# Performance work log

Hardware: AMD Instinct MI355X
Metric: run time of the kernel (lower is better)

The kernel has to match this reference:

```python
import math
import jax, jax.numpy as jnp
import numpy as np

E = 1024
H = 16
D = E // H  # head_dim = 64
B, T = 4, 2048


def setup_inputs() -> dict:
    key = jax.random.key(0)
    ks = jax.random.split(key, 9)
    s = 1.0 / math.sqrt(E)
    inp = {
        "x": jax.random.normal(ks[0], (B, T, E), dtype=jnp.float32),
        "Wq": jax.random.uniform(ks[1], (E, E), jnp.float32, -s, s),
        "bq": jax.random.uniform(ks[2], (E,), jnp.float32, -s, s),
        "Wk": jax.random.uniform(ks[3], (E, E), jnp.float32, -s, s),
        "bk": jax.random.uniform(ks[4], (E,), jnp.float32, -s, s),
        "Wv": jax.random.uniform(ks[5], (E, E), jnp.float32, -s, s),
        "bv": jax.random.uniform(ks[6], (E,), jnp.float32, -s, s),
        "Wo": jax.random.uniform(ks[7], (E, E), jnp.float32, -s, s),
        "bo": jax.random.uniform(ks[8], (E,), jnp.float32, -s, s),
    }
    return inp


def reference(x, Wq, bq, Wk, bk, Wv, bv, Wo, bo):
    # Linear projections (torch Linear: y = x @ W.T + b)
    q = x @ Wq.T + bq
    k = x @ Wk.T + bk
    v = x @ Wv.T + bv
    # [B, T, E] -> [B, H, T, D]
    def split_heads(t):
        return t.reshape(B, T, H, D).transpose(0, 2, 1, 3)
    q, k, v = split_heads(q), split_heads(k), split_heads(v)
    # scaled dot-product attention; note scale uses head_dim (attention(self.head_dim))
    scores = jnp.einsum("bhqd,bhkd->bhqk", q, k) / math.sqrt(D)
    attn = jax.nn.softmax(scores, axis=-1)
    out = jnp.einsum("bhqk,bhkd->bhqd", attn, v)
    out = out.transpose(0, 2, 1, 3).reshape(B, T, E)
    return out @ Wo.T + bo
```

## Files before the change

kernel.cpp:

```cpp
#include <hip/hip_runtime.h>

typedef short bh8 __attribute__((ext_vector_type(8)));
typedef short bh4 __attribute__((ext_vector_type(4)));
typedef float f4 __attribute__((ext_vector_type(4)));
typedef unsigned int u32;
typedef u32 u32x2 __attribute__((ext_vector_type(2)));

#if __has_builtin(__builtin_amdgcn_exp2f)
#define EXP2(x) __builtin_amdgcn_exp2f(x)
#else
#define EXP2(x) exp2f(x)
#endif

__device__ __forceinline__ short f2bf(float f) {
  unsigned u = __float_as_uint(f);
  u += 0x7FFFu + ((u >> 16) & 1u);
  return (short)(u >> 16);
}

__device__ __forceinline__ void async16(const void* g, void* l) {
  __builtin_amdgcn_global_load_lds((const __attribute__((address_space(1))) void*)g,
                                   (__attribute__((address_space(3))) void*)l, 16, 0, 0);
}

__global__ void cvt_kernel(const float* __restrict__ in, short* __restrict__ out, int n4) {
  int i = blockIdx.x * blockDim.x + threadIdx.x;
  if (i < n4) {
    f4 v = *(const f4*)(in + (size_t)i * 4);
    bh4 o;
    o[0] = f2bf(v[0]); o[1] = f2bf(v[1]); o[2] = f2bf(v[2]); o[3] = f2bf(v[3]);
    *(bh4*)(out + (size_t)i * 4) = o;
  }
}

__global__ void cvt_w4(const float* __restrict__ w0, const float* __restrict__ w1,
                       const float* __restrict__ w2, const float* __restrict__ w3,
                       short* __restrict__ out, int n4_per) {
  const float* in = blockIdx.y == 0 ? w0 : blockIdx.y == 1 ? w1 : blockIdx.y == 2 ? w2 : w3;
  short* o = out + (size_t)blockIdx.y * (size_t)n4_per * 4;
  int i = blockIdx.x * blockDim.x + threadIdx.x;
  if (i < n4_per) {
    f4 v = *(const f4*)(in + (size_t)i * 4);
    bh4 q;
    q[0] = f2bf(v[0]); q[1] = f2bf(v[1]); q[2] = f2bf(v[2]); q[3] = f2bf(v[3]);
    *(bh4*)(o + (size_t)i * 4) = q;
  }
}

template <typename OutT, bool BROW>
__device__ __forceinline__ void gemm_body(const short* __restrict__ A, const short* __restrict__ Bw,
                                          const float* __restrict__ bias, OutT* __restrict__ C,
                                          int m0, int n0, int N, int K, float scale,
                                          short* a_lds, short* b_lds) {
  const int t = threadIdx.x;
  const int lane = t & 63, wave = t >> 6, quad = lane >> 4, l15 = lane & 15;
  const int mw = (wave >> 1) * 64, nw = (wave & 1) * 64;

  f4 acc[4][4];
#pragma unroll
  for (int i = 0; i < 4; ++i)
#pragma unroll
    for (int j = 0; j < 4; ++j) acc[i][j] = (f4){0.f, 0.f, 0.f, 0.f};

  for (int k0 = 0; k0 < K; k0 += 32) {
#pragma unroll
    for (int i = 0; i < 2; ++i) {
      int c = i * 256 + t;
      int m = c >> 2;
      int kq = (c & 3) ^ ((m >> 1) & 3);
      const short* ga = A + (size_t)(m0 + m) * K + k0 + kq * 8;
      const short* gb = Bw + (size_t)(n0 + m) * K + k0 + kq * 8;
      async16(ga, (char*)a_lds + (i * 256 + wave * 64) * 16);
      async16(gb, (char*)b_lds + (i * 256 + wave * 64) * 16);
    }
    __syncthreads();
    bh8 af[4], bfr[4];
#pragma unroll
    for (int ms = 0; ms < 4; ++ms) {
      int m = mw + ms * 16 + l15;
      int pos = m * 4 + (quad ^ ((m >> 1) & 3));
      af[ms] = *(const bh8*)(a_lds + pos * 8);
    }
#pragma unroll
    for (int ns = 0; ns < 4; ++ns) {
      int n = nw + ns * 16 + l15;
      int pos = n * 4 + (quad ^ ((n >> 1) & 3));
      bfr[ns] = *(const bh8*)(b_lds + pos * 8);
    }
#pragma unroll
    for (int ms = 0; ms < 4; ++ms)
#pragma unroll
      for (int ns = 0; ns < 4; ++ns)
        acc[ms][ns] = __builtin_amdgcn_mfma_f32_16x16x32_bf16(af[ms], bfr[ns], acc[ms][ns], 0, 0, 0);
    __syncthreads();
  }
#pragma unroll
  for (int ns = 0; ns < 4; ++ns) {
    int col = n0 + nw + ns * 16 + l15;
    float bcol = BROW ? 0.f : bias[col & 1023];
#pragma unroll
    for (int ms = 0; ms < 4; ++ms) {
      int row = m0 + mw + ms * 16 + quad * 4;
      float brow = BROW ? bias[row & 1023] : 0.f;
#pragma unroll
      for (int r = 0; r < 4; ++r) {
        float bv = BROW ? bias[(row + r) & 1023] : bcol;
        float v = (acc[ms][ns][r] + bv) * scale;
        if (sizeof(OutT) == 2)
          ((short*)C)[(size_t)(row + r) * N + col] = f2bf(v);
        else
          ((float*)C)[(size_t)(row + r) * N + col] = v;
      }
      (void)brow;
    }
  }
}

__global__ void gemm_qkv(const short* __restrict__ xb, const short* __restrict__ W3,
                         const float* __restrict__ bq, const float* __restrict__ bk,
                         const float* __restrict__ bv,
                         short* __restrict__ Qo, short* __restrict__ Ko, short* __restrict__ VTo,
                         float qscale) {
  __shared__ __align__(16) short a_lds[128 * 32];
  __shared__ __align__(16) short b_lds[128 * 32];
  const int which = blockIdx.x >> 3;
  if (which == 2) {
    const short* Wv = W3 + (size_t)2 * 1024 * 1024;
    gemm_body<short, true>(Wv, xb, bv, VTo, (blockIdx.x & 7) * 128, blockIdx.y * 128,
                           8192, 1024, 1.0f, a_lds, b_lds);
  } else {
    const short* Bw = W3 + (size_t)which * 1024 * 1024;
    const float* bias = which == 0 ? bq : bk;
    short* C = which == 0 ? Qo : Ko;
    float scale = which == 0 ? qscale : 1.0f;
    gemm_body<short, false>(xb, Bw, bias, C, blockIdx.y * 128, (blockIdx.x & 7) * 128,
                            1024, 1024, scale, a_lds, b_lds);
  }
}

__global__ void gemm_bt_f32(const short* __restrict__ A, const short* __restrict__ Bw,
                            const float* __restrict__ bias, float* __restrict__ C) {
  __shared__ __align__(16) short a_lds[128 * 32];
  __shared__ __align__(16) short b_lds[128 * 32];
  gemm_body<float, false>(A, Bw, bias, C, blockIdx.y * 128, blockIdx.x * 128, 1024, 1024, 1.0f,
                          a_lds, b_lds);
}

__global__ void attn_kernel(const short* __restrict__ Qb, const short* __restrict__ Kb,
                            const short* __restrict__ VTb, short* __restrict__ AO) {
  __shared__ __align__(16) short k_lds[64 * 64];
  __shared__ __align__(16) short vt_lds[64 * 64];
  __shared__ __align__(16) short p_lds[4][32 * 72];
  const int t = threadIdx.x, lane = t & 63, wave = t >> 6, quad = lane >> 4, l15 = lane & 15;
  const int bh = blockIdx.y, b = bh >> 4, h = bh & 15;
  const int q0 = blockIdx.x * 128;
  const size_t baseq = ((size_t)b * 2048) * 1024 + (size_t)h * 64;
  const size_t basev = ((size_t)h * 64) * 8192 + (size_t)b * 2048;

  bh8 qf[2][2];
#pragma unroll
  for (int mi = 0; mi < 2; ++mi)
#pragma unroll
    for (int ks = 0; ks < 2; ++ks)
      qf[mi][ks] = *(const bh8*)(Qb + baseq + (size_t)(q0 + wave * 32 + mi * 16 + l15) * 1024 + ks * 32 + quad * 8);

  f4 O[2][4];
  float l_part[2] = {0.f, 0.f};
#pragma unroll
  for (int mi = 0; mi < 2; ++mi)
#pragma unroll
    for (int di = 0; di < 4; ++di) O[mi][di] = (f4){0.f, 0.f, 0.f, 0.f};

  for (int kt = 0; kt < 2048; kt += 64) {
    __syncthreads();
#pragma unroll
    for (int i = 0; i < 2; ++i) {
      int c = i * 256 + t;
      int kk = c >> 3;
      int dq = (c & 7) ^ (kk & 7);
      async16(Kb + baseq + (size_t)(kt + kk) * 1024 + dq * 8,
              (char*)k_lds + (i * 256 + wave * 64) * 16);
    }
#pragma unroll
    for (int i = 0; i < 2; ++i) {
      int c = i * 256 + t;
      int d = c >> 3;
      int kc = (c & 7) ^ (d & 7);
      async16(VTb + basev + (size_t)d * 8192 + kt + kc * 8,
              (char*)vt_lds + (i * 256 + wave * 64) * 16);
    }
    __syncthreads();

    f4 ST[4][2];
#pragma unroll
    for (int mK = 0; mK < 4; ++mK) {
      int key = mK * 16 + l15;
      bh8 ka0 = *(const bh8*)(k_lds + (key * 8 + (quad ^ (key & 7))) * 8);
      bh8 ka1 = *(const bh8*)(k_lds + (key * 8 + ((quad + 4) ^ (key & 7))) * 8);
#pragma unroll
      for (int mi = 0; mi < 2; ++mi) {
        f4 s = (f4){-16.f, -16.f, -16.f, -16.f};
        s = __builtin_amdgcn_mfma_f32_16x16x32_bf16(ka0, qf[mi][0], s, 0, 0, 0);
        s = __builtin_amdgcn_mfma_f32_16x16x32_bf16(ka1, qf[mi][1], s, 0, 0, 0);
        ST[mK][mi] = s;
      }
    }

#pragma unroll
    for (int mi = 0; mi < 2; ++mi) {
      float lp = 0.f;
#pragma unroll
      for (int mK = 0; mK < 4; ++mK) {
        float p0 = EXP2(ST[mK][mi][0]);
        float p1 = EXP2(ST[mK][mi][1]);
        float p2 = EXP2(ST[mK][mi][2]);
        float p3 = EXP2(ST[mK][mi][3]);
        lp += (p0 + p1) + (p2 + p3);
        u32 d0 = __builtin_amdgcn_perm(__float_as_uint(p1), __float_as_uint(p0), 0x07060302u);
        u32 d1 = __builtin_amdgcn_perm(__float_as_uint(p3), __float_as_uint(p2), 0x07060302u);
        u32x2 dd = {d0, d1};
        *(u32x2*)(&p_lds[wave][(mi * 16 + l15) * 72 + mK * 16 + quad * 4]) = dd;
      }
      l_part[mi] += lp;
    }

    bh8 pa[2][2];
#pragma unroll
    for (int mi = 0; mi < 2; ++mi)
#pragma unroll
      for (int ks = 0; ks < 2; ++ks)
        pa[mi][ks] = *(const bh8*)(&p_lds[wave][(mi * 16 + l15) * 72 + ks * 32 + quad * 8]);
#pragma unroll
    for (int di = 0; di < 4; ++di) {
      int d = di * 16 + l15;
      bh8 vb0 = *(const bh8*)(vt_lds + (d * 8 + (quad ^ (d & 7))) * 8);
      bh8 vb1 = *(const bh8*)(vt_lds + (d * 8 + ((quad + 4) ^ (d & 7))) * 8);
#pragma unroll
      for (int mi = 0; mi < 2; ++mi) {
        f4 o = O[mi][di];
        o = __builtin_amdgcn_mfma_f32_16x16x32_bf16(pa[mi][0], vb0, o, 0, 0, 0);
        o = __builtin_amdgcn_mfma_f32_16x16x32_bf16(pa[mi][1], vb1, o, 0, 0, 0);
        O[mi][di] = o;
      }
    }
  }

#pragma unroll
  for (int mi = 0; mi < 2; ++mi) {
    float l0 = l_part[mi];
    l0 += __shfl_xor(l0, 16);
    l0 += __shfl_xor(l0, 32);
    float rl[4];
#pragma unroll
    for (int r = 0; r < 4; ++r) {
      float lb = __shfl(l0, quad * 4 + r);
      rl[r] = __builtin_amdgcn_rcpf(lb);
    }
#pragma unroll
    for (int di = 0; di < 4; ++di)
#pragma unroll
      for (int r = 0; r < 4; ++r) {
        int row = q0 + wave * 32 + mi * 16 + quad * 4 + r;
        AO[baseq + (size_t)row * 1024 + di * 16 + l15] = f2bf(O[mi][di][r] * rl[r]);
      }
  }
}

extern "C" void kernel_launch(void* const* d_in, const int* in_sizes, int n_in,
                              void* d_out, int out_size, void* d_ws, size_t ws_size,
                              hipStream_t stream) {
  const float* x  = (const float*)d_in[0];
  const float* Wq = (const float*)d_in[1];
  const float* bq = (const float*)d_in[2];
  const float* Wk = (const float*)d_in[3];
  const float* bk = (const float*)d_in[4];
  const float* Wv = (const float*)d_in[5];
  const float* bv = (const float*)d_in[6];
  const float* Wo = (const float*)d_in[7];
  const float* bo = (const float*)d_in[8];
  float* out = (float*)d_out;

  const int M = 8192, E = 1024;
  const size_t NX = (size_t)M * E;
  const size_t NW = (size_t)E * E;

  short* ws  = (short*)d_ws;
  short* xb  = ws;
  short* wqb = xb + NX;
  short* wob = wqb + 3 * NW;
  short* qb  = wob + NW;
  short* kb  = qb + NX;
  short* vt  = kb + NX;
  short* aob = xb;

  cvt_kernel<<<dim3((unsigned)(NX / 1024)), 256, 0, stream>>>(x, xb, (int)(NX / 4));
  cvt_w4<<<dim3((unsigned)(NW / 1024), 4), 256, 0, stream>>>(Wq, Wk, Wv, Wo, wqb, (int)(NW / 4));

  const float qscale = 0.18033688011112042f;
  gemm_qkv<<<dim3(24, 64), 256, 0, stream>>>(xb, wqb, bq, bk, bv, qb, kb, vt, qscale);

  attn_kernel<<<dim3(16, 64), 256, 0, stream>>>(qb, kb, vt, aob);

  gemm_bt_f32<<<dim3(8, 64), 256, 0, stream>>>(aob, wob, bo, out);
}
```

Before: 281.6 us.

## Keep softmax probabilities in registers via f16 MFMA and double GEMM K-tile

The attention kernel now converts exp2 probabilities to packed fp16 in registers and feeds them straight into 16x16x16 f16 MFMAs, so the per-wave LDS round trip for P is gone. To match that, V is stored as fp16 instead of bf16 by the QKV GEMM. The GEMMs also move from a 32-wide to a 64-wide K tile with an 8-way XOR swizzle, which halves the barriers per K. The trade-offs are more LDS per block, fp16 range and precision for V and P, and twice as many smaller MFMAs for the PV product.

```diff
diff --git a/kernel.cpp b/kernel.cpp
--- a/kernel.cpp
+++ b/kernel.cpp
@@ -3,8 +3,9 @@
 typedef short bh8 __attribute__((ext_vector_type(8)));
 typedef short bh4 __attribute__((ext_vector_type(4)));
 typedef float f4 __attribute__((ext_vector_type(4)));
+typedef _Float16 fh4 __attribute__((ext_vector_type(4)));
+typedef __fp16 hp2 __attribute__((ext_vector_type(2)));
 typedef unsigned int u32;
-typedef u32 u32x2 __attribute__((ext_vector_type(2)));
 
 #if __has_builtin(__builtin_amdgcn_exp2f)
 #define EXP2(x) __builtin_amdgcn_exp2f(x)
@@ -16,6 +17,12 @@
   unsigned u = __float_as_uint(f);
   u += 0x7FFFu + ((u >> 16) & 1u);
   return (short)(u >> 16);
+}
+
+__device__ __forceinline__ short f2fh(float f) {
+  union { hp2 h2; u32 u; } cv;
+  cv.h2 = __builtin_amdgcn_cvt_pkrtz(f, f);
+  return (short)(cv.u & 0xffffu);
 }
 
 __device__ __forceinline__ void async16(const void* g, void* l) {
@@ -47,7 +54,7 @@
   }
 }
 
-template <typename OutT, bool BROW>
+template <typename OutT, bool BROW, bool F16OUT>
 __device__ __forceinline__ void gemm_body(const short* __restrict__ A, const short* __restrict__ Bw,
                                           const float* __restrict__ bias, OutT* __restrict__ C,
                                           int m0, int n0, int N, int K, float scale,
@@ -62,36 +69,39 @@
 #pragma unroll
     for (int j = 0; j < 4; ++j) acc[i][j] = (f4){0.f, 0.f, 0.f, 0.f};
 
-  for (int k0 = 0; k0 < K; k0 += 32) {
-#pragma unroll
-    for (int i = 0; i < 2; ++i) {
+  for (int k0 = 0; k0 < K; k0 += 64) {
+#pragma unroll
+    for (int i = 0; i < 4; ++i) {
       int c = i * 256 + t;
-      int m = c >> 2;
-      int kq = (c & 3) ^ ((m >> 1) & 3);
+      int m = c >> 3;
+      int kq = (c & 7) ^ (m & 7);
       const short* ga = A + (size_t)(m0 + m) * K + k0 + kq * 8;
       const short* gb = Bw + (size_t)(n0 + m) * K + k0 + kq * 8;
       async16(ga, (char*)a_lds + (i * 256 + wave * 64) * 16);
       async16(gb, (char*)b_lds + (i * 256 + wave * 64) * 16);
     }
     __syncthreads();
-    bh8 af[4], bfr[4];
-#pragma unroll
-    for (int ms = 0; ms < 4; ++ms) {
-      int m = mw + ms * 16 + l15;
-      int pos = m * 4 + (quad ^ ((m >> 1) & 3));
-      af[ms] = *(const bh8*)(a_lds + pos * 8);
-    }
-#pragma unroll
-    for (int ns = 0; ns < 4; ++ns) {
-      int n = nw + ns * 16 + l15;
-      int pos = n * 4 + (quad ^ ((n >> 1) & 3));
-      bfr[ns] = *(const bh8*)(b_lds + pos * 8);
-    }
-#pragma unroll
-    for (int ms = 0; ms < 4; ++ms)
-#pragma unroll
-      for (int ns = 0; ns < 4; ++ns)
-        acc[ms][ns] = __builtin_amdgcn_mfma_f32_16x16x32_bf16(af[ms], bfr[ns], acc[ms][ns], 0, 0, 0);
+#pragma unroll
+    for (int s = 0; s < 2; ++s) {
+      bh8 af[4], bfr[4];
+#pragma unroll
+      for (int ms = 0; ms < 4; ++ms) {
+        int m = mw + ms * 16 + l15;
+        int slot = m * 8 + ((quad + s * 4) ^ (m & 7));
+        af[ms] = *(const bh8*)(a_lds + slot * 8);
+      }
+#pragma unroll
+      for (int ns = 0; ns < 4; ++ns) {
+        int n = nw + ns * 16 + l15;
+        int slot = n * 8 + ((quad + s * 4) ^ (n & 7));
+        bfr[ns] = *(const bh8*)(b_lds + slot * 8);
+      }
+#pragma unroll
+      for (int ms = 0; ms < 4; ++ms)
+#pragma unroll
+        for (int ns = 0; ns < 4; ++ns)
+          acc[ms][ns] = __builtin_amdgcn_mfma_f32_16x16x32_bf16(af[ms], bfr[ns], acc[ms][ns], 0, 0, 0);
+    }
     __syncthreads();
   }
 #pragma unroll
@@ -101,58 +111,56 @@
 #pragma unroll
     for (int ms = 0; ms < 4; ++ms) {
       int row = m0 + mw + ms * 16 + quad * 4;
-      float brow = BROW ? bias[row & 1023] : 0.f;
 #pragma unroll
       for (int r = 0; r < 4; ++r) {
         float bv = BROW ? bias[(row + r) & 1023] : bcol;
         float v = (acc[ms][ns][r] + bv) * scale;
         if (sizeof(OutT) == 2)
-          ((short*)C)[(size_t)(row + r) * N + col] = f2bf(v);
+          ((short*)C)[(size_t)(row + r) * N + col] = F16OUT ? f2fh(v) : f2bf(v);
         else
           ((float*)C)[(size_t)(row + r) * N + col] = v;
       }
-      (void)brow;
-    }
-  }
-}
-
-__global__ void gemm_qkv(const short* __restrict__ xb, const short* __restrict__ W3,
-                         const float* __restrict__ bq, const float* __restrict__ bk,
-                         const float* __restrict__ bv,
-                         short* __restrict__ Qo, short* __restrict__ Ko, short* __restrict__ VTo,
-                         float qscale) {
-  __shared__ __align__(16) short a_lds[128 * 32];
-  __shared__ __align__(16) short b_lds[128 * 32];
+    }
+  }
+}
+
+__global__ void __launch_bounds__(256) gemm_qkv(
+    const short* __restrict__ xb, const short* __restrict__ W3,
+    const float* __restrict__ bq, const float* __restrict__ bk, const float* __restrict__ bv,
+    short* __restrict__ Qo, short* __restrict__ Ko, short* __restrict__ VTo, float qscale) {
+  __shared__ __align__(16) short a_lds[128 * 64];
+  __shared__ __align__(16) short b_lds[128 * 64];
   const int which = blockIdx.x >> 3;
   if (which == 2) {
     const short* Wv = W3 + (size_t)2 * 1024 * 1024;
-    gemm_body<short, true>(Wv, xb, bv, VTo, (blockIdx.x & 7) * 128, blockIdx.y * 128,
-                           8192, 1024, 1.0f, a_lds, b_lds);
+    gemm_body<short, true, true>(Wv, xb, bv, VTo, (blockIdx.x & 7) * 128, blockIdx.y * 128,
+                                 8192, 1024, 1.0f, a_lds, b_lds);
   } else {
     const short* Bw = W3 + (size_t)which * 1024 * 1024;
     const float* bias = which == 0 ? bq : bk;
     short* C = which == 0 ? Qo : Ko;
     float scale = which == 0 ? qscale : 1.0f;
-    gemm_body<short, false>(xb, Bw, bias, C, blockIdx.y * 128, (blockIdx.x & 7) * 128,
-                            1024, 1024, scale, a_lds, b_lds);
-  }
-}
-
-__global__ void gemm_bt_f32(const short* __restrict__ A, const short* __restrict__ Bw,
-                            const float* __restrict__ bias, float* __restrict__ C) {
-  __shared__ __align__(16) short a_lds[128 * 32];
-  __shared__ __align__(16) short b_lds[128 * 32];
-  gemm_body<float, false>(A, Bw, bias, C, blockIdx.y * 128, blockIdx.x * 128, 1024, 1024, 1.0f,
-                          a_lds, b_lds);
-}
-
-__global__ void attn_kernel(const short* __restrict__ Qb, const short* __restrict__ Kb,
-                            const short* __restrict__ VTb, short* __restrict__ AO) {
+    gemm_body<short, false, false>(xb, Bw, bias, C, blockIdx.y * 128, (blockIdx.x & 7) * 128,
+                                   1024, 1024, scale, a_lds, b_lds);
+  }
+}
+
+__global__ void __launch_bounds__(256) gemm_bt_f32(
+    const short* __restrict__ A, const short* __restrict__ Bw,
+    const float* __restrict__ bias, float* __restrict__ C) {
+  __shared__ __align__(16) short a_lds[128 * 64];
+  __shared__ __align__(16) short b_lds[128 * 64];
+  gemm_body<float, false, false>(A, Bw, bias, C, blockIdx.y * 128, blockIdx.x * 128,
+                                 1024, 1024, 1.0f, a_lds, b_lds);
+}
+
+__global__ void __launch_bounds__(256) attn_kernel(
+    const short* __restrict__ Qb, const short* __restrict__ Kb,
+    const short* __restrict__ VTb, short* __restrict__ AO) {
   __shared__ __align__(16) short k_lds[64 * 64];
   __shared__ __align__(16) short vt_lds[64 * 64];
-  __shared__ __align__(16) short p_lds[4][32 * 72];
   const int t = threadIdx.x, lane = t & 63, wave = t >> 6, quad = lane >> 4, l15 = lane & 15;
-  const int bh = blockIdx.y, b = bh >> 4, h = bh & 15;
+  const int b = blockIdx.y >> 4, h = blockIdx.y & 15;
   const int q0 = blockIdx.x * 128;
   const size_t baseq = ((size_t)b * 2048) * 1024 + (size_t)h * 64;
   const size_t basev = ((size_t)h * 64) * 8192 + (size_t)b * 2048;
@@ -206,6 +214,7 @@
       }
     }
 
+    fh4 pa[4][2];
 #pragma unroll
     for (int mi = 0; mi < 2; ++mi) {
       float lp = 0.f;
@@ -216,31 +225,26 @@
         float p2 = EXP2(ST[mK][mi][2]);
         float p3 = EXP2(ST[mK][mi][3]);
         lp += (p0 + p1) + (p2 + p3);
-        u32 d0 = __builtin_amdgcn_perm(__float_as_uint(p1), __float_as_uint(p0), 0x07060302u);
-        u32 d1 = __builtin_amdgcn_perm(__float_as_uint(p3), __float_as_uint(p2), 0x07060302u);
-        u32x2 dd = {d0, d1};
-        *(u32x2*)(&p_lds[wave][(mi * 16 + l15) * 72 + mK * 16 + quad * 4]) = dd;
+        hp2 lo = __builtin_amdgcn_cvt_pkrtz(p0, p1);
+        hp2 hi = __builtin_amdgcn_cvt_pkrtz(p2, p3);
+        fh4 pv;
+        pv[0] = (_Float16)lo[0]; pv[1] = (_Float16)lo[1];
+        pv[2] = (_Float16)hi[0]; pv[3] = (_Float16)hi[1];
+        pa[mK][mi] = pv;
       }
       l_part[mi] += lp;
     }
 
-    bh8 pa[2][2];
-#pragma unroll
-    for (int mi = 0; mi < 2; ++mi)
-#pragma unroll
-      for (int ks = 0; ks < 2; ++ks)
-        pa[mi][ks] = *(const bh8*)(&p_lds[wave][(mi * 16 + l15) * 72 + ks * 32 + quad * 8]);
 #pragma unroll
     for (int di = 0; di < 4; ++di) {
       int d = di * 16 + l15;
-      bh8 vb0 = *(const bh8*)(vt_lds + (d * 8 + (quad ^ (d & 7))) * 8);
-      bh8 vb1 = *(const bh8*)(vt_lds + (d * 8 + ((quad + 4) ^ (d & 7))) * 8);
-#pragma unroll
-      for (int mi = 0; mi < 2; ++mi) {
-        f4 o = O[mi][di];
-        o = __builtin_amdgcn_mfma_f32_16x16x32_bf16(pa[mi][0], vb0, o, 0, 0, 0);
-        o = __builtin_amdgcn_mfma_f32_16x16x32_bf16(pa[mi][1], vb1, o, 0, 0, 0);
-        O[mi][di] = o;
+#pragma unroll
+      for (int mK = 0; mK < 4; ++mK) {
+        int kc = mK * 2 + (quad >> 1);
+        fh4 vb = *(const fh4*)(vt_lds + (d * 8 + (kc ^ (d & 7))) * 8 + (quad & 1) * 4);
+#pragma unroll
+        for (int mi = 0; mi < 2; ++mi)
+          O[mi][di] = __builtin_amdgcn_mfma_f32_16x16x16f16(pa[mK][mi], vb, O[mi][di], 0, 0, 0);
       }
     }
   }
```

Result: slower. 300.6 us (+6.8%).
